# Kernel tuning notes

Hardware: AMD Instinct MI355X
Metric: run time of the kernel (lower is better)

## Reference

```python
import jax, jax.numpy as jnp
import numpy as np

HIDDEN = 4096
N_HEADS = 32
N_KV = 32
HEAD_DIM = HIDDEN // N_HEADS  # 128
T = 2048
THETA = 10000.0
EPS = 1e-5


def setup_inputs() -> dict:
    key = jax.random.key(0)
    ks = jax.random.split(key, 7)
    s = 0.02
    return {
        "positions": jnp.arange(T, dtype=jnp.int64),
        "hidden_states": jax.random.normal(ks[0], (T, HIDDEN), jnp.float32),
        "w_qkv": jax.random.normal(ks[1], ((N_HEADS + 2 * N_KV) * HEAD_DIM, HIDDEN), jnp.float32) * s,
        "w_o": jax.random.normal(ks[2], (HIDDEN, N_HEADS * HEAD_DIM), jnp.float32) * s,
        "q_norm_w": jnp.ones((N_HEADS, HEAD_DIM), jnp.float32) + jax.random.normal(ks[3], (N_HEADS, HEAD_DIM), jnp.float32) * s,
        "q_norm_b": jax.random.normal(ks[4], (N_HEADS, HEAD_DIM), jnp.float32) * s,
        "k_norm_w": jnp.ones((N_KV, HEAD_DIM), jnp.float32) + jax.random.normal(ks[5], (N_KV, HEAD_DIM), jnp.float32) * s,
        "k_norm_b": jax.random.normal(ks[6], (N_KV, HEAD_DIM), jnp.float32) * s,
    }


def _layer_norm_affine(x, w, b):
    # x: [T, H, d]; normalize over last dim, no affine inside, then per-head affine
    mu = jnp.mean(x, axis=-1, keepdims=True)
    var = jnp.var(x, axis=-1, keepdims=True)
    xn = (x - mu) * jax.lax.rsqrt(var + EPS)
    return xn * w + b


def _rope_neox(x, positions):
    # x: [T, H, d], NEOX style: rotate halves over full head_dim
    half = HEAD_DIM // 2
    inv_freq = 1.0 / (THETA ** (jnp.arange(0, half, dtype=jnp.float32) * 2.0 / HEAD_DIM))
    ang = positions.astype(jnp.float32)[:, None] * inv_freq  # [T, half]
    cos = jnp.cos(ang)[:, None, :]
    sin = jnp.sin(ang)[:, None, :]
    x1, x2 = x[..., :half], x[..., half:]
    return jnp.concatenate([x1 * cos - x2 * sin, x2 * cos + x1 * sin], axis=-1)


def reference(positions, hidden_states, w_qkv, w_o, q_norm_w, q_norm_b, k_norm_w, k_norm_b):
    qkv = hidden_states @ w_qkv.T  # [T, (H+2Hkv)*d]
    q_size = N_HEADS * HEAD_DIM
    kv_size = N_KV * HEAD_DIM
    q = qkv[:, :q_size].reshape(T, N_HEADS, HEAD_DIM)
    k = qkv[:, q_size:q_size + kv_size].reshape(T, N_KV, HEAD_DIM)
    v = qkv[:, q_size + kv_size:].reshape(T, N_KV, HEAD_DIM)

    q = _layer_norm_affine(q, q_norm_w, q_norm_b)
    k = _layer_norm_affine(k, k_norm_w, k_norm_b)
    q = _rope_neox(q, positions)
    k = _rope_neox(k, positions)

    scale = HEAD_DIM ** -0.5
    scores = jnp.einsum('thd,shd->hts', q, k) * scale  # [H, T, T]
    causal = jnp.tril(jnp.ones((T, T), dtype=bool))
    scores = jnp.where(causal[None], scores, jnp.finfo(scores.dtype).min)
    p = jax.nn.softmax(scores, axis=-1)
    attn = jnp.einsum('hts,shd->thd', p, v).reshape(T, N_HEADS * HEAD_DIM)
    return attn @ w_o.T
```

## Files before the change

### kernel.cpp

```cpp
#include <hip/hip_runtime.h>
#include <cstdint>

#define T_SEQ 2048
#define HID   4096
#define NH    32
#define HD    128
#define QKVW  12288

typedef float  f32x4  __attribute__((ext_vector_type(4)));
typedef __bf16 bf16x8 __attribute__((ext_vector_type(8)));

#define QSCALE (0.08838834764831845f * 1.4426950408889634f)

__device__ __forceinline__ unsigned short f2bf(float f) {
  unsigned int u = __builtin_bit_cast(unsigned int, f);
  u += 0x7fffu + ((u >> 16) & 1u);
  return (unsigned short)(u >> 16);
}
__device__ __forceinline__ float bf2f(unsigned short u) {
  return __builtin_bit_cast(float, (unsigned int)u << 16);
}

__device__ __forceinline__ void gload_lds16(const void* gptr, void* lptr) {
  __builtin_amdgcn_global_load_lds(
      (const __attribute__((address_space(1))) unsigned int*)(unsigned long long)(uintptr_t)gptr,
      (__attribute__((address_space(3))) unsigned int*)(unsigned int)(uintptr_t)lptr,
      16, 0, 0);
}

#define SB __builtin_amdgcn_sched_barrier(0)

__global__ __launch_bounds__(256) void cast_bf16(const float* __restrict__ in,
                                                 unsigned short* __restrict__ out,
                                                 int n4) {
  int i = blockIdx.x * 256 + threadIdx.x;
  int stride = gridDim.x * 256;
  for (; i < n4; i += stride) {
    float4 v = ((const float4*)in)[i];
    ushort4 o;
    o.x = f2bf(v.x); o.y = f2bf(v.y); o.z = f2bf(v.z); o.w = f2bf(v.w);
    ((ushort4*)out)[i] = o;
  }
}

__global__ __launch_bounds__(512, 2) void gemm_bt8(const unsigned short* __restrict__ Ag,
                                                   const unsigned short* __restrict__ Bg,
                                                   unsigned short* __restrict__ C,
                                                   int M, int N, int K, int MT) {
  __shared__ unsigned short As_[2][256 * 64];
  __shared__ unsigned short Bs_[2][192 * 64];
  const int tid  = threadIdx.x;
  const int lane = tid & 63;
  const int w    = tid >> 6;
  const int wm   = w & 3;
  const int wn   = w >> 2;
  const int l15  = lane & 15;
  const int lg   = lane >> 4;
  const int sw   = l15 & 7;

  const int cpx = gridDim.x >> 3;
  const int swz = (blockIdx.x & 7) * cpx + (blockIdx.x >> 3);
  const int bm  = (swz % MT) * 256;
  const int bn  = (swz / MT) * 192;
  const int nk  = K >> 6;

  const unsigned short* Abase = Ag + (size_t)bm * K;
  const unsigned short* Bbase = Bg + (size_t)bn * K;

#define SG(ldsbase, gbase, kt_, u_) do {                                        \
    const int _cid = (u_) * 512 + tid;                                          \
    const int _r = _cid >> 3, _ch = _cid & 7;                                   \
    gload_lds16((gbase) + (size_t)_r * K + (size_t)(kt_) * 64 +                 \
                    ((_ch ^ (_r & 7)) * 8),                                     \
                (void*)((char*)(ldsbase) + _cid * 16));                         \
  } while (0)
#define STAGE(abuf, bbuf, kt_) do {                                             \
    SG(abuf, Abase, kt_, 0); SG(abuf, Abase, kt_, 1);                           \
    SG(abuf, Abase, kt_, 2); SG(abuf, Abase, kt_, 3);                           \
    SG(bbuf, Bbase, kt_, 0); SG(bbuf, Bbase, kt_, 1);                           \
    SG(bbuf, Bbase, kt_, 2);                                                    \
  } while (0)

#define RD(base, r, kk)                                                          \
  (*(const bf16x8*)((const char*)(base) + (r) * 128 + ((((kk) * 4 + lg) ^ sw) * 16)))

#define MFMA24(afr, bfr) do {                                                    \
    _Pragma("unroll")                                                            \
    for (int _m = 0; _m < 4; ++_m)                                               \
      _Pragma("unroll")                                                          \
      for (int _n = 0; _n < 6; ++_n)                                             \
        acc[_m][_n] = __builtin_amdgcn_mfma_f32_16x16x32_bf16(                   \
            afr[_m], bfr[_n], acc[_m][_n], 0, 0, 0);                             \
  } while (0)

  f32x4 acc[4][6] = {};

  STAGE(As_[0], Bs_[0], 0);
  if (nk > 1) {
    STAGE(As_[1], Bs_[1], 1);
    asm volatile("s_waitcnt vmcnt(7)" ::: "memory");
  } else {
    asm volatile("s_waitcnt vmcnt(0)" ::: "memory");
  }
  SB;
  __builtin_amdgcn_s_barrier();

  for (int t = 0; t < nk; ++t) {
    const int cur = t & 1;
    const unsigned short* As = As_[cur];
    const unsigned short* Bs = Bs_[cur];
    bf16x8 a0[4], a1[4], b0[6], b1[6];

#pragma unroll
    for (int m = 0; m < 4; ++m) a0[m] = RD(As, wm * 64 + m * 16 + l15, 0);
#pragma unroll
    for (int n = 0; n < 6; ++n) b0[n] = RD(Bs, wn * 96 + n * 16 + l15, 0);
    SB;
#pragma unroll
    for (int m = 0; m < 4; ++m) a1[m] = RD(As, wm * 64 + m * 16 + l15, 1);
#pragma unroll
    for (int n = 0; n < 6; ++n) b1[n] = RD(Bs, wn * 96 + n * 16 + l15, 1);
    SB;
    asm volatile("s_waitcnt lgkmcnt(10)" ::: "memory");
    SB;
    __builtin_amdgcn_s_setprio(1);
    MFMA24(a0, b0);
    __builtin_amdgcn_s_setprio(0);
    SB;
    asm volatile("s_waitcnt lgkmcnt(0)" ::: "memory");
    SB;
    __builtin_amdgcn_s_barrier();
    if (t + 2 < nk) STAGE(As_[cur], Bs_[cur], t + 2);
    SB;
    __builtin_amdgcn_s_setprio(1);
    MFMA24(a1, b1);
    __builtin_amdgcn_s_setprio(0);
    if (t + 1 < nk) {
      if (t + 2 < nk) asm volatile("s_waitcnt vmcnt(7)" ::: "memory");
      else            asm volatile("s_waitcnt vmcnt(0)" ::: "memory");
      SB;
      __builtin_amdgcn_s_barrier();
    }
  }
#undef SG
#undef STAGE
#undef RD
#undef MFMA24

#pragma unroll
  for (int m = 0; m < 4; ++m)
#pragma unroll
    for (int i = 0; i < 4; ++i) {
      const int row = bm + wm * 64 + m * 16 + lg * 4 + i;
#pragma unroll
      for (int n = 0; n < 6; ++n)
        C[(size_t)row * N + bn + wn * 96 + n * 16 + l15] = f2bf(acc[m][n][i]);
    }
}

__global__ __launch_bounds__(512, 2) void gemm2_bt8(const unsigned short* __restrict__ Ag,
                                                    const unsigned short* __restrict__ Bg,
                                                    float* __restrict__ C,
                                                    int M, int N, int K, int MT) {
  __shared__ unsigned short As_[2][256 * 64];
  __shared__ unsigned short Bs_[2][128 * 64];
  const int tid  = threadIdx.x;
  const int lane = tid & 63;
  const int w    = tid >> 6;
  const int wm   = w & 3;
  const int wn   = w >> 2;
  const int l15  = lane & 15;
  const int lg   = lane >> 4;
  const int sw   = l15 & 7;

  const int cpx = gridDim.x >> 3;
  const int swz = (blockIdx.x & 7) * cpx + (blockIdx.x >> 3);
  const int bm  = (swz % MT) * 256;
  const int bn  = (swz / MT) * 128;
  const int nk  = K >> 6;

  const unsigned short* Abase = Ag + (size_t)bm * K;
  const unsigned short* Bbase = Bg + (size_t)bn * K;

#define SG(ldsbase, gbase, kt_, u_) do {                                        \
    const int _cid = (u_) * 512 + tid;                                          \
    const int _r = _cid >> 3, _ch = _cid & 7;                                   \
    gload_lds16((gbase) + (size_t)_r * K + (size_t)(kt_) * 64 +                 \
                    ((_ch ^ (_r & 7)) * 8),                                     \
                (void*)((char*)(ldsbase) + _cid * 16));                         \
  } while (0)
#define STAGE(abuf, bbuf, kt_) do {                                             \
    SG(abuf, Abase, kt_, 0); SG(abuf, Abase, kt_, 1);                           \
    SG(abuf, Abase, kt_, 2); SG(abuf, Abase, kt_, 3);                           \
    SG(bbuf, Bbase, kt_, 0); SG(bbuf, Bbase, kt_, 1);                           \
  } while (0)

#define RD(base, r, kk)                                                          \
  (*(const bf16x8*)((const char*)(base) + (r) * 128 + ((((kk) * 4 + lg) ^ sw) * 16)))

#define MFMA16(afr, bfr) do {                                                    \
    _Pragma("unroll")                                                            \
    for (int _m = 0; _m < 4; ++_m)                                               \
      _Pragma("unroll")                                                          \
      for (int _n = 0; _n < 4; ++_n)                                             \
        acc[_m][_n] = __builtin_amdgcn_mfma_f32_16x16x32_bf16(                   \
            afr[_m], bfr[_n], acc[_m][_n], 0, 0, 0);                             \
  } while (0)

  f32x4 acc[4][4] = {};

  STAGE(As_[0], Bs_[0], 0);
  if (nk > 1) {
    STAGE(As_[1], Bs_[1], 1);
    asm volatile("s_waitcnt vmcnt(6)" ::: "memory");
  } else {
    asm volatile("s_waitcnt vmcnt(0)" ::: "memory");
  }
  SB;
  __builtin_amdgcn_s_barrier();

  for (int t = 0; t < nk; ++t) {
    const int cur = t & 1;
    const unsigned short* As = As_[cur];
    const unsigned short* Bs = Bs_[cur];
    bf16x8 a0[4], a1[4], b0[4], b1[4];

#pragma unroll
    for (int m = 0; m < 4; ++m) a0[m] = RD(As, wm * 64 + m * 16 + l15, 0);
#pragma unroll
    for (int n = 0; n < 4; ++n) b0[n] = RD(Bs, wn * 64 + n * 16 + l15, 0);
    SB;
#pragma unroll
    for (int m = 0; m < 4; ++m) a1[m] = RD(As, wm * 64 + m * 16 + l15, 1);
#pragma unroll
    for (int n = 0; n < 4; ++n) b1[n] = RD(Bs, wn * 64 + n * 16 + l15, 1);
    SB;
    asm volatile("s_waitcnt lgkmcnt(8)" ::: "memory");
    SB;
    __builtin_amdgcn_s_setprio(1);
    MFMA16(a0, b0);
    __builtin_amdgcn_s_setprio(0);
    SB;
    asm volatile("s_waitcnt lgkmcnt(0)" ::: "memory");
    SB;
    __builtin_amdgcn_s_barrier();
    if (t + 2 < nk) STAGE(As_[cur], Bs_[cur], t + 2);
    SB;
    __builtin_amdgcn_s_setprio(1);
    MFMA16(a1, b1);
    __builtin_amdgcn_s_setprio(0);
    if (t + 1 < nk) {
      if (t + 2 < nk) asm volatile("s_waitcnt vmcnt(6)" ::: "memory");
      else            asm volatile("s_waitcnt vmcnt(0)" ::: "memory");
      SB;
      __builtin_amdgcn_s_barrier();
    }
  }
#undef SG
#undef STAGE
#undef RD
#undef MFMA16

#pragma unroll
  for (int m = 0; m < 4; ++m)
#pragma unroll
    for (int i = 0; i < 4; ++i) {
      const int row = bm + wm * 64 + m * 16 + lg * 4 + i;
#pragma unroll
      for (int n = 0; n < 4; ++n)
        C[(size_t)row * N + bn + wn * 64 + n * 16 + l15] = acc[m][n][i];
    }
}

__global__ __launch_bounds__(256) void norm_rope(const unsigned short* __restrict__ qkv,
                                                 const float* __restrict__ qw,
                                                 const float* __restrict__ qb,
                                                 const float* __restrict__ kw,
                                                 const float* __restrict__ kb,
                                                 unsigned short* __restrict__ q,
                                                 unsigned short* __restrict__ k) {
  const int t    = blockIdx.x;
  const int tid  = threadIdx.x;
  const int lane = tid & 63;
  const int w    = tid >> 6;
  const float invf = exp2f(-(float)lane * (13.287712379549449f / 64.0f));
  const float ang  = (float)t * invf;
  const float c = cosf(ang), s = sinf(ang);
  const unsigned short* row = qkv + (size_t)t * QKVW;

#pragma unroll 1
  for (int sel = 0; sel < 2; ++sel) {
    const unsigned short* src = row + sel * HID;
    const float* wgt = sel ? kw : qw;
    const float* bia = sel ? kb : qb;
    unsigned short* dst = sel ? k : q;
    const float oscale = sel ? 1.0f : QSCALE;
    for (int h = w; h < NH; h += 4) {
      const unsigned short* x = src + h * HD;
      float x1 = bf2f(x[lane]), x2 = bf2f(x[lane + 64]);
      float sum = x1 + x2, ss = x1 * x1 + x2 * x2;
#pragma unroll
      for (int m = 1; m < 64; m <<= 1) {
        sum += __shfl_xor(sum, m, 64);
        ss  += __shfl_xor(ss, m, 64);
      }
      const float mu  = sum * (1.0f / 128.0f);
      const float var = ss * (1.0f / 128.0f) - mu * mu;
      const float r   = rsqrtf(var + 1e-5f);
      const float n1  = (x1 - mu) * r * wgt[h * HD + lane]      + bia[h * HD + lane];
      const float n2  = (x2 - mu) * r * wgt[h * HD + lane + 64] + bia[h * HD + lane + 64];
      const float o1  = (n1 * c - n2 * s) * oscale;
      const float o2  = (n2 * c + n1 * s) * oscale;
      dst[(size_t)t * HID + h * HD + lane]      = f2bf(o1);
      dst[(size_t)t * HID + h * HD + lane + 64] = f2bf(o2);
    }
  }
}

__global__ __launch_bounds__(256) void transpose_v(const unsigned short* __restrict__ v,
                                                   unsigned short* __restrict__ vt) {
  __shared__ unsigned short tile[64][65];
  const int h  = blockIdx.z;
  const int tt = blockIdx.x * 64;
  const int dd = blockIdx.y * 64;
  const int tid = threadIdx.x;
#pragma unroll
  for (int p = 0; p < 4; ++p) {
    int idx = p * 256 + tid;
    int r = idx >> 4, c4 = idx & 15;
    ushort4 val = *(const ushort4*)&v[(size_t)(tt + r) * QKVW + h * HD + dd + c4 * 4];
    tile[r][c4 * 4 + 0] = val.x;
    tile[r][c4 * 4 + 1] = val.y;
    tile[r][c4 * 4 + 2] = val.z;
    tile[r][c4 * 4 + 3] = val.w;
  }
  __syncthreads();
#pragma unroll
  for (int p = 0; p < 4; ++p) {
    int idx = p * 256 + tid;
    int r = idx >> 4, c4 = idx & 15;
    ushort4 o;
    o.x = tile[c4 * 4 + 0][r];
    o.y = tile[c4 * 4 + 1][r];
    o.z = tile[c4 * 4 + 2][r];
    o.w = tile[c4 * 4 + 3][r];
    *(ushort4*)&vt[((size_t)h * HD + dd + r) * T_SEQ + tt + c4 * 4] = o;
  }
}

__global__ __launch_bounds__(256) void attn_fwd(const unsigned short* __restrict__ Q,
                                                const unsigned short* __restrict__ K,
                                                const unsigned short* __restrict__ VT,
                                                unsigned short* __restrict__ O) {
  __shared__ unsigned short Ks[2][64 * 128];
  __shared__ unsigned short Vs[2][128 * 64];
  __shared__ unsigned short Ps[4][16 * 64];
  const int h    = blockIdx.y;
  const int pair = blockIdx.x;
  const int tid  = threadIdx.x;
  const int lane = tid & 63;
  const int w    = tid >> 6;
  const int l15  = lane & 15;
  const int lg   = lane >> 4;
  const int sw   = l15 & 7;

#pragma unroll 1
  for (int half = 0; half < 2; ++half) {
    const int qt   = half ? (31 - pair) : pair;
    const int qrow = qt * 64 + w * 16;

    bf16x8 qf[4];
#pragma unroll
    for (int kk = 0; kk < 4; ++kk)
      qf[kk] = *(const bf16x8*)&Q[(size_t)(qrow + l15) * HID + h * HD + kk * 32 + lg * 8];

    f32x4 o[8] = {};
    float mrow[4], lrow[4];
#pragma unroll
    for (int i = 0; i < 4; ++i) { mrow[i] = -1e30f; lrow[i] = 0.0f; }

    const int nkt = qt + 1;

    {
#pragma unroll
      for (int p = 0; p < 4; ++p) {
        const int c  = p * 256 + tid;
        const int kr = c >> 4, kc = c & 15;
        gload_lds16(&K[(size_t)kr * HID + h * HD + ((kc ^ (kr & 7)) * 8)],
                    &Ks[0][(p * 256 + w * 64) * 8]);
        const int vr = c >> 3, vc = c & 7;
        gload_lds16(&VT[((size_t)h * HD + vr) * T_SEQ + ((vc ^ (vr & 7)) * 8)],
                    &Vs[0][(p * 256 + w * 64) * 8]);
      }
    }
    __syncthreads();

#pragma unroll 1
    for (int kt = 0; kt < nkt; ++kt) {
      const int cur = kt & 1;
      if (kt + 1 < nkt) {
        const int k0 = (kt + 1) * 64;
#pragma unroll
        for (int p = 0; p < 4; ++p) {
          const int c  = p * 256 + tid;
          const int kr = c >> 4, kc = c & 15;
          gload_lds16(&K[(size_t)(k0 + kr) * HID + h * HD + ((kc ^ (kr & 7)) * 8)],
                      &Ks[cur ^ 1][(p * 256 + w * 64) * 8]);
          const int vr = c >> 3, vc = c & 7;
          gload_lds16(&VT[((size_t)h * HD + vr) * T_SEQ + k0 + ((vc ^ (vr & 7)) * 8)],
                      &Vs[cur ^ 1][(p * 256 + w * 64) * 8]);
        }
      }
      const unsigned short* ksb = Ks[cur];
      const unsigned short* vsb = Vs[cur];

      f32x4 sfr[4] = {};
#pragma unroll
      for (int n = 0; n < 4; ++n)
#pragma unroll
        for (int kk = 0; kk < 4; ++kk) {
          bf16x8 kf = *(const bf16x8*)&ksb[(n * 16 + l15) * 128 + ((kk * 4 + lg) ^ sw) * 8];
          sfr[n] = __builtin_amdgcn_mfma_f32_16x16x32_bf16(qf[kk], kf, sfr[n], 0, 0, 0);
        }

      if (kt == qt) {
#pragma unroll
        for (int n = 0; n < 4; ++n)
#pragma unroll
          for (int i = 0; i < 4; ++i)
            if (n * 16 + l15 > w * 16 + lg * 4 + i) sfr[n][i] = -1e30f;
      }

      float escale[4];
#pragma unroll
      for (int i = 0; i < 4; ++i) {
        float mx = fmaxf(fmaxf(sfr[0][i], sfr[1][i]), fmaxf(sfr[2][i], sfr[3][i]));
        mx = fmaxf(mx, __shfl_xor(mx, 1, 64));
        mx = fmaxf(mx, __shfl_xor(mx, 2, 64));
        mx = fmaxf(mx, __shfl_xor(mx, 4, 64));
        mx = fmaxf(mx, __shfl_xor(mx, 8, 64));
        const float mnew = fmaxf(mrow[i], mx);
        escale[i] = exp2f(mrow[i] - mnew);
        mrow[i] = mnew;
        const int prow = lg * 4 + i;
        float rs = 0.0f;
#pragma unroll
        for (int n = 0; n < 4; ++n) {
          const float p = exp2f(sfr[n][i] - mnew);
          rs += p;
          Ps[w][prow * 64 + (((2 * n + (l15 >> 3)) ^ (prow & 7)) * 8) + sw] = f2bf(p);
        }
        rs += __shfl_xor(rs, 1, 64);
        rs += __shfl_xor(rs, 2, 64);
        rs += __shfl_xor(rs, 4, 64);
        rs += __shfl_xor(rs, 8, 64);
        lrow[i] = lrow[i] * escale[i] + rs;
      }
#pragma unroll
      for (int f = 0; f < 8; ++f)
#pragma unroll
        for (int i = 0; i < 4; ++i) o[f][i] *= escale[i];

      asm volatile("s_waitcnt lgkmcnt(0)" ::: "memory");
      __builtin_amdgcn_sched_barrier(0);

      bf16x8 pf[2];
#pragma unroll
      for (int kk = 0; kk < 2; ++kk)
        pf[kk] = *(const bf16x8*)&Ps[w][l15 * 64 + ((kk * 4 + lg) ^ sw) * 8];
#pragma unroll
      for (int f = 0; f < 8; ++f)
#pragma unroll
        for (int kk = 0; kk < 2; ++kk) {
          bf16x8 vf = *(const bf16x8*)&vsb[(f * 16 + l15) * 64 + ((kk * 4 + lg) ^ sw) * 8];
          o[f] = __builtin_amdgcn_mfma_f32_16x16x32_bf16(pf[kk], vf, o[f], 0, 0, 0);
        }

      __syncthreads();
    }

#pragma unroll
    for (int i = 0; i < 4; ++i) {
      const float inv = 1.0f / lrow[i];
      const int trow = qrow + lg * 4 + i;
#pragma unroll
      for (int f = 0; f < 8; ++f)
        O[(size_t)trow * HID + h * HD + f * 16 + l15] = f2bf(o[f][i] * inv);
    }
  }
}

extern "C" void kernel_launch(void* const* d_in, const int* in_sizes, int n_in,
                              void* d_out, int out_size, void* d_ws, size_t ws_size,
                              hipStream_t stream) {
  const float* hidden = (const float*)d_in[1];
  const float* w_qkv  = (const float*)d_in[2];
  const float* w_o    = (const float*)d_in[3];
  const float* qw     = (const float*)d_in[4];
  const float* qb     = (const float*)d_in[5];
  const float* kw     = (const float*)d_in[6];
  const float* kb     = (const float*)d_in[7];

  char* ws = (char*)d_ws;
  unsigned short* wqkv_bf = (unsigned short*)(ws + 0);
  unsigned short* attn_bf = (unsigned short*)(ws + 0);
  unsigned short* wo_bf   = (unsigned short*)(ws + 16777216);
  unsigned short* hid_bf  = (unsigned short*)(ws + 100663296);
  unsigned short* vt_bf   = (unsigned short*)(ws + 100663296);
  unsigned short* qkv_bf  = (unsigned short*)(ws + 117440512);
  unsigned short* q_bf    = (unsigned short*)(ws + 167772160);
  unsigned short* k_bf    = (unsigned short*)(ws + 184549376);

  cast_bf16<<<2048, 256, 0, stream>>>(hidden, hid_bf, (T_SEQ * HID) / 4);
  cast_bf16<<<2048, 256, 0, stream>>>(w_qkv, wqkv_bf, (QKVW * HID) / 4);
  gemm_bt8<<<512, 512, 0, stream>>>(hid_bf, wqkv_bf, qkv_bf, T_SEQ, QKVW, HID, 8);
  cast_bf16<<<2048, 256, 0, stream>>>(w_o, wo_bf, (HID * HID) / 4);
  norm_rope<<<T_SEQ, 256, 0, stream>>>(qkv_bf, qw, qb, kw, kb, q_bf, k_bf);
  transpose_v<<<dim3(T_SEQ / 64, HD / 64, NH), 256, 0, stream>>>(qkv_bf + 2 * HID, vt_bf);
  attn_fwd<<<dim3(16, NH), 256, 0, stream>>>(q_bf, k_bf, vt_bf, attn_bf);
  gemm2_bt8<<<256, 512, 0, stream>>>(attn_bf, wo_bf, (float*)d_out, T_SEQ, HID, HID, 8);
}
```

Before: 459.0 us.

## Fuse fp32-to-bf16 weight casts into GEMM B-tile loading

Drops the separate cast kernels for w_qkv and w_o. The two GEMMs now read fp32 weights directly into registers, convert them with packed bf16 conversion instructions, and store them into LDS, with the register-staged loads pipelined one tile ahead. This removes a full read and write of both weight matrices (about 256MB fp32 read plus 128MB bf16 write) and two kernel launches. In exchange, each GEMM reads twice the B bytes per tile (fp32), repeatedly across M tiles, and moves B loads from direct-to-LDS to register staging with extra VGPR and LDS store pressure.

```diff
diff --git a/kernel.cpp b/kernel.cpp
--- a/kernel.cpp
+++ b/kernel.cpp
@@ -29,6 +29,14 @@
 }
 
 #define SB __builtin_amdgcn_sched_barrier(0)
+
+__device__ __forceinline__ void cvt_store8(void* lds, float4 v) {
+  unsigned int lo, hi;
+  asm("v_cvt_pk_bf16_f32 %0, %1, %2" : "=v"(lo) : "v"(v.x), "v"(v.y));
+  asm("v_cvt_pk_bf16_f32 %0, %1, %2" : "=v"(hi) : "v"(v.z), "v"(v.w));
+  uint2 p; p.x = lo; p.y = hi;
+  *(uint2*)lds = p;
+}
 
 __global__ __launch_bounds__(256) void cast_bf16(const float* __restrict__ in,
                                                  unsigned short* __restrict__ out,
@@ -44,7 +52,7 @@
 }
 
 __global__ __launch_bounds__(512, 2) void gemm_bt8(const unsigned short* __restrict__ Ag,
-                                                   const unsigned short* __restrict__ Bg,
+                                                   const float* __restrict__ Bg,
                                                    unsigned short* __restrict__ C,
                                                    int M, int N, int K, int MT) {
   __shared__ unsigned short As_[2][256 * 64];
@@ -65,20 +73,37 @@
   const int nk  = K >> 6;
 
   const unsigned short* Abase = Ag + (size_t)bm * K;
-  const unsigned short* Bbase = Bg + (size_t)bn * K;
-
-#define SG(ldsbase, gbase, kt_, u_) do {                                        \
-    const int _cid = (u_) * 512 + tid;                                          \
-    const int _r = _cid >> 3, _ch = _cid & 7;                                   \
-    gload_lds16((gbase) + (size_t)_r * K + (size_t)(kt_) * 64 +                 \
-                    ((_ch ^ (_r & 7)) * 8),                                     \
-                (void*)((char*)(ldsbase) + _cid * 16));                         \
+  const float*          Bbase = Bg + (size_t)bn * K;
+
+  int bofs[6], blds[6];
+#pragma unroll
+  for (int j = 0; j < 6; ++j) {
+    const int hid = j * 512 + tid;
+    const int cid = hid >> 1, hh = hid & 1;
+    const int r = cid >> 3, ch = cid & 7;
+    bofs[j] = r * K + ((ch ^ (r & 7)) * 8 + hh * 4);
+    blds[j] = cid * 16 + hh * 8;
+  }
+  float4 btmp[6];
+
+#define AST(buf, kt_) do {                                                      \
+    _Pragma("unroll")                                                           \
+    for (int _u = 0; _u < 4; ++_u) {                                            \
+      const int _cid = _u * 512 + tid;                                          \
+      const int _r = _cid >> 3, _ch = _cid & 7;                                 \
+      gload_lds16(Abase + (size_t)_r * K + (size_t)(kt_) * 64 +                 \
+                      ((_ch ^ (_r & 7)) * 8),                                   \
+                  (void*)((char*)(buf) + _cid * 16));                           \
+    } } while (0)
+#define BLOAD(kt_) do {                                                         \
+    _Pragma("unroll")                                                           \
+    for (int _j = 0; _j < 6; ++_j)                                              \
+      btmp[_j] = *(const float4*)(Bbase + (size_t)(kt_) * 64 + bofs[_j]);       \
   } while (0)
-#define STAGE(abuf, bbuf, kt_) do {                                             \
-    SG(abuf, Abase, kt_, 0); SG(abuf, Abase, kt_, 1);                           \
-    SG(abuf, Abase, kt_, 2); SG(abuf, Abase, kt_, 3);                           \
-    SG(bbuf, Bbase, kt_, 0); SG(bbuf, Bbase, kt_, 1);                           \
-    SG(bbuf, Bbase, kt_, 2);                                                    \
+#define BSTORE(buf) do {                                                        \
+    _Pragma("unroll")                                                           \
+    for (int _j = 0; _j < 6; ++_j)                                              \
+      cvt_store8((char*)(buf) + blds[_j], btmp[_j]);                            \
   } while (0)
 
 #define RD(base, r, kk)                                                          \
@@ -95,13 +120,15 @@
 
   f32x4 acc[4][6] = {};
 
-  STAGE(As_[0], Bs_[0], 0);
-  if (nk > 1) {
-    STAGE(As_[1], Bs_[1], 1);
-    asm volatile("s_waitcnt vmcnt(7)" ::: "memory");
-  } else {
-    asm volatile("s_waitcnt vmcnt(0)" ::: "memory");
-  }
+  BLOAD(0); SB;
+  AST(As_[0], 0); SB;
+  asm volatile("s_waitcnt vmcnt(4)" ::: "memory");
+  SB;
+  BSTORE(Bs_[0]); SB;
+  BLOAD(1); SB;
+  AST(As_[1], 1); SB;
+  asm volatile("s_waitcnt vmcnt(10)" ::: "memory");
+  asm volatile("s_waitcnt lgkmcnt(0)" ::: "memory");
   SB;
   __builtin_amdgcn_s_barrier();
 
@@ -111,6 +138,8 @@
     const unsigned short* Bs = Bs_[cur];
     bf16x8 a0[4], a1[4], b0[6], b1[6];
 
+    if (t + 1 < nk) { BSTORE(Bs_[cur ^ 1]); SB; }
+
 #pragma unroll
     for (int m = 0; m < 4; ++m) a0[m] = RD(As, wm * 64 + m * 16 + l15, 0);
 #pragma unroll
@@ -130,20 +159,20 @@
     asm volatile("s_waitcnt lgkmcnt(0)" ::: "memory");
     SB;
     __builtin_amdgcn_s_barrier();
-    if (t + 2 < nk) STAGE(As_[cur], Bs_[cur], t + 2);
-    SB;
+    if (t + 2 < nk) { BLOAD(t + 2); SB; AST(As_[cur], t + 2); SB; }
     __builtin_amdgcn_s_setprio(1);
     MFMA24(a1, b1);
     __builtin_amdgcn_s_setprio(0);
     if (t + 1 < nk) {
-      if (t + 2 < nk) asm volatile("s_waitcnt vmcnt(7)" ::: "memory");
+      if (t + 2 < nk) asm volatile("s_waitcnt vmcnt(10)" ::: "memory");
       else            asm volatile("s_waitcnt vmcnt(0)" ::: "memory");
       SB;
       __builtin_amdgcn_s_barrier();
     }
   }
-#undef SG
-#undef STAGE
+#undef AST
+#undef BLOAD
+#undef BSTORE
 #undef RD
 #undef MFMA24
 
@@ -159,7 +188,7 @@
 }
 
 __global__ __launch_bounds__(512, 2) void gemm2_bt8(const unsigned short* __restrict__ Ag,
-                                                    const unsigned short* __restrict__ Bg,
+                                                    const float* __restrict__ Bg,
                                                     float* __restrict__ C,
                                                     int M, int N, int K, int MT) {
   __shared__ unsigned short As_[2][256 * 64];
@@ -180,19 +209,37 @@
   const int nk  = K >> 6;
 
   const unsigned short* Abase = Ag + (size_t)bm * K;
-  const unsigned short* Bbase = Bg + (size_t)bn * K;
-
-#define SG(ldsbase, gbase, kt_, u_) do {                                        \
-    const int _cid = (u_) * 512 + tid;                                          \
-    const int _r = _cid >> 3, _ch = _cid & 7;                                   \
-    gload_lds16((gbase) + (size_t)_r * K + (size_t)(kt_) * 64 +                 \
-                    ((_ch ^ (_r & 7)) * 8),                                     \
-                (void*)((char*)(ldsbase) + _cid * 16));                         \
+  const float*          Bbase = Bg + (size_t)bn * K;
+
+  int bofs[4], blds[4];
+#pragma unroll
+  for (int j = 0; j < 4; ++j) {
+    const int hid = j * 512 + tid;
+    const int cid = hid >> 1, hh = hid & 1;
+    const int r = cid >> 3, ch = cid & 7;
+    bofs[j] = r * K + ((ch ^ (r & 7)) * 8 + hh * 4);
+    blds[j] = cid * 16 + hh * 8;
+  }
+  float4 btmp[4];
+
+#define AST(buf, kt_) do {                                                      \
+    _Pragma("unroll")                                                           \
+    for (int _u = 0; _u < 4; ++_u) {                                            \
+      const int _cid = _u * 512 + tid;                                          \
+      const int _r = _cid >> 3, _ch = _cid & 7;                                 \
+      gload_lds16(Abase + (size_t)_r * K + (size_t)(kt_) * 64 +                 \
+                      ((_ch ^ (_r & 7)) * 8),                                   \
+                  (void*)((char*)(buf) + _cid * 16));                           \
+    } } while (0)
+#define BLOAD(kt_) do {                                                         \
+    _Pragma("unroll")                                                           \
+    for (int _j = 0; _j < 4; ++_j)                                              \
+      btmp[_j] = *(const float4*)(Bbase + (size_t)(kt_) * 64 + bofs[_j]);       \
   } while (0)
-#define STAGE(abuf, bbuf, kt_) do {                                             \
-    SG(abuf, Abase, kt_, 0); SG(abuf, Abase, kt_, 1);                           \
-    SG(abuf, Abase, kt_, 2); SG(abuf, Abase, kt_, 3);                           \
-    SG(bbuf, Bbase, kt_, 0); SG(bbuf, Bbase, kt_, 1);                           \
+#define BSTORE(buf) do {                                                        \
+    _Pragma("unroll")                                                           \
+    for (int _j = 0; _j < 4; ++_j)                                              \
+      cvt_store8((char*)(buf) + blds[_j], btmp[_j]);                            \
   } while (0)
 
 #define RD(base, r, kk)                                                          \
@@ -209,13 +256,15 @@
 
   f32x4 acc[4][4] = {};
 
-  STAGE(As_[0], Bs_[0], 0);
-  if (nk > 1) {
-    STAGE(As_[1], Bs_[1], 1);
-    asm volatile("s_waitcnt vmcnt(6)" ::: "memory");
-  } else {
-    asm volatile("s_waitcnt vmcnt(0)" ::: "memory");
-  }
+  BLOAD(0); SB;
+  AST(As_[0], 0); SB;
+  asm volatile("s_waitcnt vmcnt(4)" ::: "memory");
+  SB;
+  BSTORE(Bs_[0]); SB;
+  BLOAD(1); SB;
+  AST(As_[1], 1); SB;
+  asm volatile("s_waitcnt vmcnt(8)" ::: "memory");
+  asm volatile("s_waitcnt lgkmcnt(0)" ::: "memory");
   SB;
   __builtin_amdgcn_s_barrier();
 
@@ -225,6 +274,8 @@
     const unsigned short* Bs = Bs_[cur];
     bf16x8 a0[4], a1[4], b0[4], b1[4];
 
+    if (t + 1 < nk) { BSTORE(Bs_[cur ^ 1]); SB; }
+
 #pragma unroll
     for (int m = 0; m < 4; ++m) a0[m] = RD(As, wm * 64 + m * 16 + l15, 0);
 #pragma unroll
@@ -244,20 +295,20 @@
     asm volatile("s_waitcnt lgkmcnt(0)" ::: "memory");
     SB;
     __builtin_amdgcn_s_barrier();
-    if (t + 2 < nk) STAGE(As_[cur], Bs_[cur], t + 2);
-    SB;
+    if (t + 2 < nk) { BLOAD(t + 2); SB; AST(As_[cur], t + 2); SB; }
     __builtin_amdgcn_s_setprio(1);
     MFMA16(a1, b1);
     __builtin_amdgcn_s_setprio(0);
     if (t + 1 < nk) {
-      if (t + 2 < nk) asm volatile("s_waitcnt vmcnt(6)" ::: "memory");
+      if (t + 2 < nk) asm volatile("s_waitcnt vmcnt(8)" ::: "memory");
       else            asm volatile("s_waitcnt vmcnt(0)" ::: "memory");
       SB;
       __builtin_amdgcn_s_barrier();
     }
   }
-#undef SG
-#undef STAGE
+#undef AST
+#undef BLOAD
+#undef BSTORE
 #undef RD
 #undef MFMA16
 
@@ -502,21 +553,17 @@
   const float* kb     = (const float*)d_in[7];
 
   char* ws = (char*)d_ws;
-  unsigned short* wqkv_bf = (unsigned short*)(ws + 0);
   unsigned short* attn_bf = (unsigned short*)(ws + 0);
-  unsigned short* wo_bf   = (unsigned short*)(ws + 16777216);
-  unsigned short* hid_bf  = (unsigned short*)(ws + 100663296);
-  unsigned short* vt_bf   = (unsigned short*)(ws + 100663296);
-  unsigned short* qkv_bf  = (unsigned short*)(ws + 117440512);
-  unsigned short* q_bf    = (unsigned short*)(ws + 167772160);
-  unsigned short* k_bf    = (unsigned short*)(ws + 184549376);
+  unsigned short* hid_bf  = (unsigned short*)(ws + 16777216);
+  unsigned short* vt_bf   = (unsigned short*)(ws + 33554432);
+  unsigned short* qkv_bf  = (unsigned short*)(ws + 50331648);
+  unsigned short* q_bf    = (unsigned short*)(ws + 100663296);
+  unsigned short* k_bf    = (unsigned short*)(ws + 117440512);
 
   cast_bf16<<<2048, 256, 0, stream>>>(hidden, hid_bf, (T_SEQ * HID) / 4);
-  cast_bf16<<<2048, 256, 0, stream>>>(w_qkv, wqkv_bf, (QKVW * HID) / 4);
-  gemm_bt8<<<512, 512, 0, stream>>>(hid_bf, wqkv_bf, qkv_bf, T_SEQ, QKVW, HID, 8);
-  cast_bf16<<<2048, 256, 0, stream>>>(w_o, wo_bf, (HID * HID) / 4);
+  gemm_bt8<<<512, 512, 0, stream>>>(hid_bf, w_qkv, qkv_bf, T_SEQ, QKVW, HID, 8);
   norm_rope<<<T_SEQ, 256, 0, stream>>>(qkv_bf, qw, qb, kw, kb, q_bf, k_bf);
   transpose_v<<<dim3(T_SEQ / 64, HD / 64, NH), 256, 0, stream>>>(qkv_bf + 2 * HID, vt_bf);
   attn_fwd<<<dim3(16, NH), 256, 0, stream>>>(q_bf, k_bf, vt_bf, attn_bf);
-  gemm2_bt8<<<256, 512, 0, stream>>>(attn_bf, wo_bf, (float*)d_out, T_SEQ, HID, HID, 8);
-}
+  gemm2_bt8<<<256, 512, 0, stream>>>(attn_bf, w_o, (float*)d_out, T_SEQ, HID, HID, 8);
+}
```

Result: slower. 508.3 us (+10.7%).

## Fuse fp32-to-bf16 weight cast into QKV GEMM B-operand loading

Applied to the files above, without the earlier changes.

Removes the separate cast kernel for w_qkv. The QKV GEMM now loads fp32 weights through registers, converts them with packed bf16 conversion instructions and stores them into LDS, using a three-deep register prefetch with a reworked waitcnt schedule. This saves writing and re-reading a 100MB bf16 weight copy. In exchange the B operand now travels through VGPRs instead of direct-to-LDS loads, and because each output tile re-reads the fp32 weights, the GEMM moves more global memory per tile.

```diff
diff --git a/kernel.cpp b/kernel.cpp
--- a/kernel.cpp
+++ b/kernel.cpp
@@ -29,6 +29,14 @@
 }
 
 #define SB __builtin_amdgcn_sched_barrier(0)
+
+__device__ __forceinline__ void cvt_store8(void* lds, float4 v) {
+  unsigned int lo, hi;
+  asm("v_cvt_pk_bf16_f32 %0, %1, %2" : "=v"(lo) : "v"(v.x), "v"(v.y));
+  asm("v_cvt_pk_bf16_f32 %0, %1, %2" : "=v"(hi) : "v"(v.z), "v"(v.w));
+  uint2 p; p.x = lo; p.y = hi;
+  *(uint2*)lds = p;
+}
 
 __global__ __launch_bounds__(256) void cast_bf16(const float* __restrict__ in,
                                                  unsigned short* __restrict__ out,
@@ -44,7 +52,7 @@
 }
 
 __global__ __launch_bounds__(512, 2) void gemm_bt8(const unsigned short* __restrict__ Ag,
-                                                   const unsigned short* __restrict__ Bg,
+                                                   const float* __restrict__ Bg,
                                                    unsigned short* __restrict__ C,
                                                    int M, int N, int K, int MT) {
   __shared__ unsigned short As_[2][256 * 64];
@@ -65,20 +73,37 @@
   const int nk  = K >> 6;
 
   const unsigned short* Abase = Ag + (size_t)bm * K;
-  const unsigned short* Bbase = Bg + (size_t)bn * K;
-
-#define SG(ldsbase, gbase, kt_, u_) do {                                        \
-    const int _cid = (u_) * 512 + tid;                                          \
-    const int _r = _cid >> 3, _ch = _cid & 7;                                   \
-    gload_lds16((gbase) + (size_t)_r * K + (size_t)(kt_) * 64 +                 \
-                    ((_ch ^ (_r & 7)) * 8),                                     \
-                (void*)((char*)(ldsbase) + _cid * 16));                         \
-  } while (0)
-#define STAGE(abuf, bbuf, kt_) do {                                             \
-    SG(abuf, Abase, kt_, 0); SG(abuf, Abase, kt_, 1);                           \
-    SG(abuf, Abase, kt_, 2); SG(abuf, Abase, kt_, 3);                           \
-    SG(bbuf, Bbase, kt_, 0); SG(bbuf, Bbase, kt_, 1);                           \
-    SG(bbuf, Bbase, kt_, 2);                                                    \
+  const float*          Bbase = Bg + (size_t)bn * K;
+
+  int bofs[6], blds[6];
+#pragma unroll
+  for (int j = 0; j < 6; ++j) {
+    const int hid = j * 512 + tid;
+    const int cid = hid >> 1, hh = hid & 1;
+    const int r = cid >> 3, ch = cid & 7;
+    bofs[j] = r * K + ((ch ^ (r & 7)) * 8 + hh * 4);
+    blds[j] = cid * 16 + hh * 8;
+  }
+  float4 btmp0[6], btmp1[6];
+
+#define AST(buf, kt_) do {                                                      \
+    _Pragma("unroll")                                                           \
+    for (int _u = 0; _u < 4; ++_u) {                                            \
+      const int _cid = _u * 512 + tid;                                          \
+      const int _r = _cid >> 3, _ch = _cid & 7;                                 \
+      gload_lds16(Abase + (size_t)_r * K + (size_t)(kt_) * 64 +                 \
+                      ((_ch ^ (_r & 7)) * 8),                                   \
+                  (void*)((char*)(buf) + _cid * 16));                           \
+    } } while (0)
+#define BLOAD(kt_, BX) do {                                                     \
+    _Pragma("unroll")                                                           \
+    for (int _j = 0; _j < 6; ++_j)                                              \
+      BX[_j] = *(const float4*)(Bbase + (size_t)(kt_) * 64 + bofs[_j]);         \
+  } while (0)
+#define BSTORE(buf, BX) do {                                                    \
+    _Pragma("unroll")                                                           \
+    for (int _j = 0; _j < 6; ++_j)                                              \
+      cvt_store8((char*)(buf) + blds[_j], BX[_j]);                              \
   } while (0)
 
 #define RD(base, r, kk)                                                          \
@@ -95,55 +120,67 @@
 
   f32x4 acc[4][6] = {};
 
-  STAGE(As_[0], Bs_[0], 0);
-  if (nk > 1) {
-    STAGE(As_[1], Bs_[1], 1);
-    asm volatile("s_waitcnt vmcnt(7)" ::: "memory");
-  } else {
-    asm volatile("s_waitcnt vmcnt(0)" ::: "memory");
-  }
+  BLOAD(0, btmp0); SB;
+  AST(As_[0], 0); SB;
+  asm volatile("s_waitcnt vmcnt(4)" ::: "memory");
+  SB;
+  BSTORE(Bs_[0], btmp0); SB;
+  BLOAD(1, btmp1); SB;
+  AST(As_[1], 1); SB;
+  BLOAD(2, btmp0); SB;
+  asm volatile("s_waitcnt vmcnt(16)" ::: "memory");
+  asm volatile("s_waitcnt lgkmcnt(0)" ::: "memory");
   SB;
   __builtin_amdgcn_s_barrier();
 
-  for (int t = 0; t < nk; ++t) {
-    const int cur = t & 1;
-    const unsigned short* As = As_[cur];
-    const unsigned short* Bs = Bs_[cur];
-    bf16x8 a0[4], a1[4], b0[6], b1[6];
-
-#pragma unroll
-    for (int m = 0; m < 4; ++m) a0[m] = RD(As, wm * 64 + m * 16 + l15, 0);
-#pragma unroll
-    for (int n = 0; n < 6; ++n) b0[n] = RD(Bs, wn * 96 + n * 16 + l15, 0);
-    SB;
-#pragma unroll
-    for (int m = 0; m < 4; ++m) a1[m] = RD(As, wm * 64 + m * 16 + l15, 1);
-#pragma unroll
-    for (int n = 0; n < 6; ++n) b1[n] = RD(Bs, wn * 96 + n * 16 + l15, 1);
-    SB;
-    asm volatile("s_waitcnt lgkmcnt(10)" ::: "memory");
-    SB;
-    __builtin_amdgcn_s_setprio(1);
-    MFMA24(a0, b0);
-    __builtin_amdgcn_s_setprio(0);
-    SB;
-    asm volatile("s_waitcnt lgkmcnt(0)" ::: "memory");
-    SB;
-    __builtin_amdgcn_s_barrier();
-    if (t + 2 < nk) STAGE(As_[cur], Bs_[cur], t + 2);
-    SB;
-    __builtin_amdgcn_s_setprio(1);
-    MFMA24(a1, b1);
-    __builtin_amdgcn_s_setprio(0);
-    if (t + 1 < nk) {
-      if (t + 2 < nk) asm volatile("s_waitcnt vmcnt(7)" ::: "memory");
-      else            asm volatile("s_waitcnt vmcnt(0)" ::: "memory");
-      SB;
-      __builtin_amdgcn_s_barrier();
-    }
-  }
-#undef SG
-#undef STAGE
+#define KTILE(t_, BX) do {                                                      \
+    const int _t = (t_);                                                        \
+    const int _cur = _t & 1;                                                    \
+    const unsigned short* As = As_[_cur];                                       \
+    const unsigned short* Bs = Bs_[_cur];                                       \
+    bf16x8 a0[4], a1[4], b0[6], b1[6];                                          \
+    if (_t + 1 < nk) { BSTORE(Bs_[_cur ^ 1], BX); SB; }                         \
+    _Pragma("unroll")                                                           \
+    for (int m = 0; m < 4; ++m) a0[m] = RD(As, wm * 64 + m * 16 + l15, 0);      \
+    _Pragma("unroll")                                                           \
+    for (int n = 0; n < 6; ++n) b0[n] = RD(Bs, wn * 96 + n * 16 + l15, 0);      \
+    SB;                                                                         \
+    _Pragma("unroll")                                                           \
+    for (int m = 0; m < 4; ++m) a1[m] = RD(As, wm * 64 + m * 16 + l15, 1);      \
+    _Pragma("unroll")                                                           \
+    for (int n = 0; n < 6; ++n) b1[n] = RD(Bs, wn * 96 + n * 16 + l15, 1);      \
+    SB;                                                                         \
+    asm volatile("s_waitcnt lgkmcnt(10)" ::: "memory");                         \
+    SB;                                                                         \
+    __builtin_amdgcn_s_setprio(1);                                              \
+    MFMA24(a0, b0);                                                             \
+    __builtin_amdgcn_s_setprio(0);                                              \
+    SB;                                                                         \
+    asm volatile("s_waitcnt lgkmcnt(0)" ::: "memory");                          \
+    SB;                                                                         \
+    __builtin_amdgcn_s_barrier();                                               \
+    if (_t + 3 < nk) { BLOAD(_t + 3, BX); SB; }                                 \
+    if (_t + 2 < nk) { AST(As_[_cur], _t + 2); SB; }                            \
+    __builtin_amdgcn_s_setprio(1);                                              \
+    MFMA24(a1, b1);                                                             \
+    __builtin_amdgcn_s_setprio(0);                                              \
+    if (_t + 1 < nk) {                                                          \
+      if (_t + 3 < nk)      asm volatile("s_waitcnt vmcnt(10)" ::: "memory");   \
+      else if (_t + 2 < nk) asm volatile("s_waitcnt vmcnt(4)" ::: "memory");    \
+      else                  asm volatile("s_waitcnt vmcnt(0)" ::: "memory");    \
+      SB;                                                                       \
+      __builtin_amdgcn_s_barrier();                                             \
+    }                                                                           \
+  } while (0)
+
+  for (int t = 0; t < nk; t += 2) {
+    KTILE(t, btmp1);
+    KTILE(t + 1, btmp0);
+  }
+#undef KTILE
+#undef AST
+#undef BLOAD
+#undef BSTORE
 #undef RD
 #undef MFMA24
 
@@ -502,18 +539,16 @@
   const float* kb     = (const float*)d_in[7];
 
   char* ws = (char*)d_ws;
-  unsigned short* wqkv_bf = (unsigned short*)(ws + 0);
   unsigned short* attn_bf = (unsigned short*)(ws + 0);
   unsigned short* wo_bf   = (unsigned short*)(ws + 16777216);
-  unsigned short* hid_bf  = (unsigned short*)(ws + 100663296);
-  unsigned short* vt_bf   = (unsigned short*)(ws + 100663296);
-  unsigned short* qkv_bf  = (unsigned short*)(ws + 117440512);
-  unsigned short* q_bf    = (unsigned short*)(ws + 167772160);
-  unsigned short* k_bf    = (unsigned short*)(ws + 184549376);
+  unsigned short* hid_bf  = (unsigned short*)(ws + 50331648);
+  unsigned short* vt_bf   = (unsigned short*)(ws + 67108864);
+  unsigned short* qkv_bf  = (unsigned short*)(ws + 83886080);
+  unsigned short* q_bf    = (unsigned short*)(ws + 134217728);
+  unsigned short* k_bf    = (unsigned short*)(ws + 150994944);
 
   cast_bf16<<<2048, 256, 0, stream>>>(hidden, hid_bf, (T_SEQ * HID) / 4);
-  cast_bf16<<<2048, 256, 0, stream>>>(w_qkv, wqkv_bf, (QKVW * HID) / 4);
-  gemm_bt8<<<512, 512, 0, stream>>>(hid_bf, wqkv_bf, qkv_bf, T_SEQ, QKVW, HID, 8);
+  gemm_bt8<<<512, 512, 0, stream>>>(hid_bf, w_qkv, qkv_bf, T_SEQ, QKVW, HID, 8);
   cast_bf16<<<2048, 256, 0, stream>>>(w_o, wo_bf, (HID * HID) / 4);
   norm_rope<<<T_SEQ, 256, 0, stream>>>(qkv_bf, qw, qb, kw, kb, q_bf, k_bf);
   transpose_v<<<dim3(T_SEQ / 64, HD / 64, NH), 256, 0, stream>>>(qkv_bf + 2 * HID, vt_bf);
```

New measurement: 1.020 ms. 2.22x slower.
